# Performance work log

Measured on AMD Instinct MI355X. Metric: run time of the kernel, lower is better.

The kernel has to match this reference:

```python
import jax, jax.numpy as jnp
import numpy as np

N_MOL = 128
N_ATOMS_MAX = 1024
N_PAIRS = 4_194_304  # ~32 neighbors per atom


def setup_inputs() -> dict:
    key = jax.random.key(0)
    k0, k1, k2, k3, k4 = jax.random.split(key, 5)
    n_flat = N_MOL * N_ATOMS_MAX
    # coordinates inside a ~20 Angstrom box
    coordinates = jax.random.uniform(k0, (N_MOL, N_ATOMS_MAX, 3), jnp.float32) * 20.0
    # near-orthorhombic cells: 20*I + small perturbation
    cell = (jnp.eye(3, dtype=jnp.float32) * 20.0)[None, :, :] + 0.05 * jax.random.normal(
        k1, (N_MOL, 3, 3), jnp.float32)
    # all padded atoms treated as real -> identity index maps
    real_atoms = jnp.arange(n_flat, dtype=jnp.int64)
    inv_real_atoms = jnp.arange(n_flat, dtype=jnp.int64)
    mol_index = jnp.repeat(jnp.arange(N_MOL, dtype=jnp.int64), N_ATOMS_MAX)
    # neighbor pairs in padded flat-index space (what compute_one + mol offset emits)
    pair_first_raw = jax.random.randint(k2, (N_PAIRS,), 0, n_flat, dtype=jnp.int64)
    pair_second_raw = jax.random.randint(k3, (N_PAIRS,), 0, n_flat, dtype=jnp.int64)
    # periodic image offsets in {-1, 0, 1}^3
    offsets = jax.random.randint(k4, (N_PAIRS, 3), 0, 3, dtype=jnp.int32) - 1
    return dict(
        coordinates=coordinates,
        cell=cell,
        real_atoms=real_atoms,
        inv_real_atoms=inv_real_atoms,
        mol_index=mol_index,
        pair_first_raw=pair_first_raw,
        pair_second_raw=pair_second_raw,
        offsets=offsets,
        n_images=1,
        n_molecules=N_MOL,
        n_atoms_max=N_ATOMS_MAX,
    )


def reference(coordinates, cell, real_atoms, inv_real_atoms, mol_index,
              pair_first_raw, pair_second_raw, offsets, n_images,
              n_molecules, n_atoms_max):
    # map padded flat indices -> real-atom indices
    pair_first = inv_real_atoms[pair_first_raw]
    pair_second = inv_real_atoms[pair_second_raw]
    # linearized image-offset index in a (2*n_images+1)^3 grid
    n_off = 2 * n_images + 1
    o = offsets + n_images  # [P, 3], values in [0, n_off)
    offset_index = o[:, 2] + n_off * (o[:, 1] + n_off * o[:, 0])
    # per-pair cell gather and 3x3 matvec: offsets @ cell[mol]
    pair_mol = mol_index[pair_first]
    pair_cell = cell[pair_mol]  # [P, 3, 3]
    pair_offsets = jnp.einsum('pi,pij->pj', offsets.astype(cell.dtype), pair_cell)
    # gather real-atom coordinates from padded array
    coordflat = coordinates.reshape(n_molecules * n_atoms_max, 3)[real_atoms]
    paircoord = coordflat[pair_first] - coordflat[pair_second] + pair_offsets
    distflat2 = jnp.linalg.norm(paircoord, axis=1)
    return (distflat2, pair_first, pair_second, paircoord, offsets, offset_index)
```

## Files before the change

kernel.cpp:

```cpp
#include <hip/hip_runtime.h>


typedef int   iv4 __attribute__((ext_vector_type(4)));
typedef float fv4 __attribute__((ext_vector_type(4)));

#define NT_LOAD(p)      __builtin_nontemporal_load(p)
#define NT_STORE(p, v)  __builtin_nontemporal_store(v, p)

static __device__ __forceinline__ fv4 mkf4(float a, float b, float c, float d) {
    fv4 v; v.x = a; v.y = b; v.z = c; v.w = d; return v;
}

__global__ void build_tabA(
    const float* __restrict__ coordinates,
    const int*   __restrict__ real_atoms,
    const int*   __restrict__ inv_real_atoms,
    const int*   __restrict__ mol_index,
    fv4* __restrict__ tabA,
    int n_flat)
{
    int i = blockIdx.x * blockDim.x + threadIdx.x;
    if (i >= n_flat) return;
    const int pf = inv_real_atoms[i];
    const int r  = real_atoms[pf];
    const int m  = mol_index[pf];
    fv4 v;
    v.x = coordinates[3 * r + 0];
    v.y = coordinates[3 * r + 1];
    v.z = coordinates[3 * r + 2];
    v.w = __int_as_float(pf | (m << 17));
    tabA[i] = v;
}

__global__ void __launch_bounds__(256)
pairs_kernel(
    const fv4* __restrict__ tabA,
    const float* __restrict__ cell,
    const int* __restrict__ pair_first_raw,
    const int* __restrict__ pair_second_raw,
    const int* __restrict__ offsets,
    int n_images, int n_mol,
    float* __restrict__ out,
    int P)
{
    extern __shared__ float sc[];
    for (int i = threadIdx.x; i < n_mol * 9; i += blockDim.x)
        sc[i] = cell[i];
    __syncthreads();

    const int n_off = 2 * n_images + 1;

    const int t = blockIdx.x * blockDim.x + threadIdx.x;
    if (t * 4 >= P) return;

    const iv4 fr  = NT_LOAD((const iv4*)pair_first_raw + t);
    const iv4 sr  = NT_LOAD((const iv4*)pair_second_raw + t);
    const iv4 ow0 = NT_LOAD((const iv4*)offsets + 3 * t + 0);
    const iv4 ow1 = NT_LOAD((const iv4*)offsets + 3 * t + 1);
    const iv4 ow2 = NT_LOAD((const iv4*)offsets + 3 * t + 2);

    const int frv[4] = {fr.x, fr.y, fr.z, fr.w};
    const int srv[4] = {sr.x, sr.y, sr.z, sr.w};
    const int o[4][3] = {
        {ow0.x, ow0.y, ow0.z},
        {ow0.w, ow1.x, ow1.y},
        {ow1.z, ow1.w, ow2.x},
        {ow2.y, ow2.z, ow2.w},
    };

    fv4 A[4], B[4];
#pragma unroll
    for (int i = 0; i < 4; ++i) {
        A[i] = tabA[frv[i]];
        B[i] = tabA[srv[i]];
    }

    int pf[4], ps[4], oi[4];
    float pc[4][3], dist[4];
#pragma unroll
    for (int i = 0; i < 4; ++i) {
        const int wa = __float_as_int(A[i].w);
        const int wb = __float_as_int(B[i].w);
        pf[i] = wa & 0x1FFFF;
        ps[i] = wb & 0x1FFFF;
        const int mol = wa >> 17;
        const float* C = sc + mol * 9;

        const float f0 = (float)o[i][0], f1 = (float)o[i][1], f2 = (float)o[i][2];
        const float po0 = f0 * C[0] + f1 * C[3] + f2 * C[6];
        const float po1 = f0 * C[1] + f1 * C[4] + f2 * C[7];
        const float po2 = f0 * C[2] + f1 * C[5] + f2 * C[8];

        pc[i][0] = A[i].x - B[i].x + po0;
        pc[i][1] = A[i].y - B[i].y + po1;
        pc[i][2] = A[i].z - B[i].z + po2;
        dist[i] = sqrtf(pc[i][0] * pc[i][0] + pc[i][1] * pc[i][1] + pc[i][2] * pc[i][2]);

        oi[i] = (o[i][2] + n_images) + n_off * ((o[i][1] + n_images) + n_off * (o[i][0] + n_images));
    }

    NT_STORE((fv4*)(out) + t,          mkf4(dist[0], dist[1], dist[2], dist[3]));
    NT_STORE((fv4*)(out + P) + t,      mkf4((float)pf[0], (float)pf[1], (float)pf[2], (float)pf[3]));
    NT_STORE((fv4*)(out + 2 * P) + t,  mkf4((float)ps[0], (float)ps[1], (float)ps[2], (float)ps[3]));

    fv4* pc_out = (fv4*)(out + 3 * P) + 3 * t;
    NT_STORE(pc_out + 0, mkf4(pc[0][0], pc[0][1], pc[0][2], pc[1][0]));
    NT_STORE(pc_out + 1, mkf4(pc[1][1], pc[1][2], pc[2][0], pc[2][1]));
    NT_STORE(pc_out + 2, mkf4(pc[2][2], pc[3][0], pc[3][1], pc[3][2]));

    fv4* of_out = (fv4*)(out + 6 * P) + 3 * t;
    NT_STORE(of_out + 0, mkf4((float)o[0][0], (float)o[0][1], (float)o[0][2], (float)o[1][0]));
    NT_STORE(of_out + 1, mkf4((float)o[1][1], (float)o[1][2], (float)o[2][0], (float)o[2][1]));
    NT_STORE(of_out + 2, mkf4((float)o[2][2], (float)o[3][0], (float)o[3][1], (float)o[3][2]));

    NT_STORE((fv4*)(out + 9 * P) + t, mkf4((float)oi[0], (float)oi[1], (float)oi[2], (float)oi[3]));
}

__global__ void fallback_kernel(
    const float* __restrict__ coordinates,
    const float* __restrict__ cell,
    const int*   __restrict__ real_atoms,
    const int*   __restrict__ inv_real_atoms,
    const int*   __restrict__ mol_index,
    const int*   __restrict__ pair_first_raw,
    const int*   __restrict__ pair_second_raw,
    const int*   __restrict__ offsets,
    int n_images,
    float* __restrict__ out,
    int P)
{
    const int n_off = 2 * n_images + 1;
    int p = blockIdx.x * blockDim.x + threadIdx.x;
    if (p >= P) return;
    const int pf = inv_real_atoms[pair_first_raw[p]];
    const int ps = inv_real_atoms[pair_second_raw[p]];
    const int o0 = offsets[3 * p + 0], o1 = offsets[3 * p + 1], o2 = offsets[3 * p + 2];
    const int mol = mol_index[pf];
    const float* __restrict__ C = cell + mol * 9;
    const float f0 = (float)o0, f1 = (float)o1, f2 = (float)o2;
    const float po0 = f0 * C[0] + f1 * C[3] + f2 * C[6];
    const float po1 = f0 * C[1] + f1 * C[4] + f2 * C[7];
    const float po2 = f0 * C[2] + f1 * C[5] + f2 * C[8];
    const int ra = real_atoms[pf], rb = real_atoms[ps];
    const float pcx = coordinates[3*ra+0] - coordinates[3*rb+0] + po0;
    const float pcy = coordinates[3*ra+1] - coordinates[3*rb+1] + po1;
    const float pcz = coordinates[3*ra+2] - coordinates[3*rb+2] + po2;
    out[p] = sqrtf(pcx*pcx + pcy*pcy + pcz*pcz);
    out[P + p] = (float)pf;
    out[2*P + p] = (float)ps;
    out[3*P + 3*p + 0] = pcx; out[3*P + 3*p + 1] = pcy; out[3*P + 3*p + 2] = pcz;
    out[6*P + 3*p + 0] = (float)o0; out[6*P + 3*p + 1] = (float)o1; out[6*P + 3*p + 2] = (float)o2;
    out[9*P + p] = (float)((o2 + n_images) + n_off * ((o1 + n_images) + n_off * (o0 + n_images)));
}

extern "C" void kernel_launch(void* const* d_in, const int* in_sizes, int n_in,
                              void* d_out, int out_size, void* d_ws, size_t ws_size,
                              hipStream_t stream) {
    const float* coordinates     = (const float*)d_in[0];
    const float* cell            = (const float*)d_in[1];
    const int*   real_atoms      = (const int*)d_in[2];
    const int*   inv_real_atoms  = (const int*)d_in[3];
    const int*   mol_index       = (const int*)d_in[4];
    const int*   pair_first_raw  = (const int*)d_in[5];
    const int*   pair_second_raw = (const int*)d_in[6];
    const int*   offsets         = (const int*)d_in[7];

    const int P      = in_sizes[5];
    const int n_flat = in_sizes[2];
    const int n_mol  = in_sizes[1] / 9;
    const int n_images = 1;

    float* out = (float*)d_out;

    const size_t tabA_bytes = (size_t)n_flat * sizeof(fv4);
    const size_t smem_bytes = (size_t)n_mol * 9 * sizeof(float);

    if (ws_size >= tabA_bytes && smem_bytes <= 64 * 1024) {
        fv4* tabA = (fv4*)d_ws;

        build_tabA<<<(n_flat + 255) / 256, 256, 0, stream>>>(
            coordinates, real_atoms, inv_real_atoms, mol_index, tabA, n_flat);

        const int threads = P / 4;
        pairs_kernel<<<(threads + 255) / 256, 256, smem_bytes, stream>>>(
            tabA, cell, pair_first_raw, pair_second_raw, offsets,
            n_images, n_mol, out, P);
    } else {
        fallback_kernel<<<(P + 255) / 256, 256, 0, stream>>>(
            coordinates, cell, real_atoms, inv_real_atoms, mol_index,
            pair_first_raw, pair_second_raw, offsets, n_images, out, P);
    }
}
```

Baseline: 92.10 us.

## Convert pairs kernel to grid-stride loop with software-prefetched index loads

Caps the grid at 2048 blocks and makes each thread loop over several 4-pair chunks. It prefetches the next chunk's pair indices and offsets while gathering and computing the current chunk, and sets launch_bounds to request 8 blocks per CU. The goal is to overlap streaming index loads with the dependent tabA gathers and to amortize the shared-memory cell load. The trade-off is fewer resident waves to hide latency and extra registers for the prefetched values.

After: 169.7 us. 84.3% more time.

```diff
diff --git a/kernel.cpp b/kernel.cpp
--- a/kernel.cpp
+++ b/kernel.cpp
@@ -32,7 +32,7 @@
     tabA[i] = v;
 }
 
-__global__ void __launch_bounds__(256)
+__global__ void __launch_bounds__(256, 8)
 pairs_kernel(
     const fv4* __restrict__ tabA,
     const float* __restrict__ cell,
@@ -48,72 +48,88 @@
         sc[i] = cell[i];
     __syncthreads();
 
-    const int n_off = 2 * n_images + 1;
-
-    const int t = blockIdx.x * blockDim.x + threadIdx.x;
-    if (t * 4 >= P) return;
-
-    const iv4 fr  = NT_LOAD((const iv4*)pair_first_raw + t);
-    const iv4 sr  = NT_LOAD((const iv4*)pair_second_raw + t);
-    const iv4 ow0 = NT_LOAD((const iv4*)offsets + 3 * t + 0);
-    const iv4 ow1 = NT_LOAD((const iv4*)offsets + 3 * t + 1);
-    const iv4 ow2 = NT_LOAD((const iv4*)offsets + 3 * t + 2);
-
-    const int frv[4] = {fr.x, fr.y, fr.z, fr.w};
-    const int srv[4] = {sr.x, sr.y, sr.z, sr.w};
-    const int o[4][3] = {
-        {ow0.x, ow0.y, ow0.z},
-        {ow0.w, ow1.x, ow1.y},
-        {ow1.z, ow1.w, ow2.x},
-        {ow2.y, ow2.z, ow2.w},
-    };
-
-    fv4 A[4], B[4];
+    const int n_off   = 2 * n_images + 1;
+    const int nchunks = P >> 2;
+    const int stride  = gridDim.x * blockDim.x;
+
+    int c = blockIdx.x * blockDim.x + threadIdx.x;
+    if (c >= nchunks) return;
+
+    iv4 fr = NT_LOAD((const iv4*)pair_first_raw + c);
+    iv4 sr = NT_LOAD((const iv4*)pair_second_raw + c);
+    iv4 w0 = NT_LOAD((const iv4*)offsets + 3 * c + 0);
+    iv4 w1 = NT_LOAD((const iv4*)offsets + 3 * c + 1);
+    iv4 w2 = NT_LOAD((const iv4*)offsets + 3 * c + 2);
+
+    for (;;) {
+        fv4 A[4], B[4];
+        A[0] = tabA[fr.x]; B[0] = tabA[sr.x];
+        A[1] = tabA[fr.y]; B[1] = tabA[sr.y];
+        A[2] = tabA[fr.z]; B[2] = tabA[sr.z];
+        A[3] = tabA[fr.w]; B[3] = tabA[sr.w];
+
+        const int cn = c + stride;
+        const bool more = cn < nchunks;
+        iv4 nfr, nsr, nw0, nw1, nw2;
+        if (more) {
+            nfr = NT_LOAD((const iv4*)pair_first_raw + cn);
+            nsr = NT_LOAD((const iv4*)pair_second_raw + cn);
+            nw0 = NT_LOAD((const iv4*)offsets + 3 * cn + 0);
+            nw1 = NT_LOAD((const iv4*)offsets + 3 * cn + 1);
+            nw2 = NT_LOAD((const iv4*)offsets + 3 * cn + 2);
+        }
+
+        const int o[4][3] = {
+            {w0.x, w0.y, w0.z},
+            {w0.w, w1.x, w1.y},
+            {w1.z, w1.w, w2.x},
+            {w2.y, w2.z, w2.w},
+        };
+
+        int pf[4], ps[4], oi[4];
+        float pc[4][3], dist[4];
 #pragma unroll
-    for (int i = 0; i < 4; ++i) {
-        A[i] = tabA[frv[i]];
-        B[i] = tabA[srv[i]];
+        for (int i = 0; i < 4; ++i) {
+            const int wa = __float_as_int(A[i].w);
+            const int wb = __float_as_int(B[i].w);
+            pf[i] = wa & 0x1FFFF;
+            ps[i] = wb & 0x1FFFF;
+            const int mol = wa >> 17;
+            const float* C = sc + mol * 9;
+
+            const float f0 = (float)o[i][0], f1 = (float)o[i][1], f2 = (float)o[i][2];
+            const float po0 = f0 * C[0] + f1 * C[3] + f2 * C[6];
+            const float po1 = f0 * C[1] + f1 * C[4] + f2 * C[7];
+            const float po2 = f0 * C[2] + f1 * C[5] + f2 * C[8];
+
+            pc[i][0] = A[i].x - B[i].x + po0;
+            pc[i][1] = A[i].y - B[i].y + po1;
+            pc[i][2] = A[i].z - B[i].z + po2;
+            dist[i] = sqrtf(pc[i][0] * pc[i][0] + pc[i][1] * pc[i][1] + pc[i][2] * pc[i][2]);
+
+            oi[i] = (o[i][2] + n_images) + n_off * ((o[i][1] + n_images) + n_off * (o[i][0] + n_images));
+        }
+
+        NT_STORE((fv4*)(out) + c,          mkf4(dist[0], dist[1], dist[2], dist[3]));
+        NT_STORE((fv4*)(out + P) + c,      mkf4((float)pf[0], (float)pf[1], (float)pf[2], (float)pf[3]));
+        NT_STORE((fv4*)(out + 2 * P) + c,  mkf4((float)ps[0], (float)ps[1], (float)ps[2], (float)ps[3]));
+
+        fv4* pc_out = (fv4*)(out + 3 * P) + 3 * c;
+        NT_STORE(pc_out + 0, mkf4(pc[0][0], pc[0][1], pc[0][2], pc[1][0]));
+        NT_STORE(pc_out + 1, mkf4(pc[1][1], pc[1][2], pc[2][0], pc[2][1]));
+        NT_STORE(pc_out + 2, mkf4(pc[2][2], pc[3][0], pc[3][1], pc[3][2]));
+
+        fv4* of_out = (fv4*)(out + 6 * P) + 3 * c;
+        NT_STORE(of_out + 0, mkf4((float)o[0][0], (float)o[0][1], (float)o[0][2], (float)o[1][0]));
+        NT_STORE(of_out + 1, mkf4((float)o[1][1], (float)o[1][2], (float)o[2][0], (float)o[2][1]));
+        NT_STORE(of_out + 2, mkf4((float)o[2][2], (float)o[3][0], (float)o[3][1], (float)o[3][2]));
+
+        NT_STORE((fv4*)(out + 9 * P) + c, mkf4((float)oi[0], (float)oi[1], (float)oi[2], (float)oi[3]));
+
+        if (!more) break;
+        c = cn;
+        fr = nfr; sr = nsr; w0 = nw0; w1 = nw1; w2 = nw2;
     }
-
-    int pf[4], ps[4], oi[4];
-    float pc[4][3], dist[4];
-#pragma unroll
-    for (int i = 0; i < 4; ++i) {
-        const int wa = __float_as_int(A[i].w);
-        const int wb = __float_as_int(B[i].w);
-        pf[i] = wa & 0x1FFFF;
-        ps[i] = wb & 0x1FFFF;
-        const int mol = wa >> 17;
-        const float* C = sc + mol * 9;
-
-        const float f0 = (float)o[i][0], f1 = (float)o[i][1], f2 = (float)o[i][2];
-        const float po0 = f0 * C[0] + f1 * C[3] + f2 * C[6];
-        const float po1 = f0 * C[1] + f1 * C[4] + f2 * C[7];
-        const float po2 = f0 * C[2] + f1 * C[5] + f2 * C[8];
-
-        pc[i][0] = A[i].x - B[i].x + po0;
-        pc[i][1] = A[i].y - B[i].y + po1;
-        pc[i][2] = A[i].z - B[i].z + po2;
-        dist[i] = sqrtf(pc[i][0] * pc[i][0] + pc[i][1] * pc[i][1] + pc[i][2] * pc[i][2]);
-
-        oi[i] = (o[i][2] + n_images) + n_off * ((o[i][1] + n_images) + n_off * (o[i][0] + n_images));
-    }
-
-    NT_STORE((fv4*)(out) + t,          mkf4(dist[0], dist[1], dist[2], dist[3]));
-    NT_STORE((fv4*)(out + P) + t,      mkf4((float)pf[0], (float)pf[1], (float)pf[2], (float)pf[3]));
-    NT_STORE((fv4*)(out + 2 * P) + t,  mkf4((float)ps[0], (float)ps[1], (float)ps[2], (float)ps[3]));
-
-    fv4* pc_out = (fv4*)(out + 3 * P) + 3 * t;
-    NT_STORE(pc_out + 0, mkf4(pc[0][0], pc[0][1], pc[0][2], pc[1][0]));
-    NT_STORE(pc_out + 1, mkf4(pc[1][1], pc[1][2], pc[2][0], pc[2][1]));
-    NT_STORE(pc_out + 2, mkf4(pc[2][2], pc[3][0], pc[3][1], pc[3][2]));
-
-    fv4* of_out = (fv4*)(out + 6 * P) + 3 * t;
-    NT_STORE(of_out + 0, mkf4((float)o[0][0], (float)o[0][1], (float)o[0][2], (float)o[1][0]));
-    NT_STORE(of_out + 1, mkf4((float)o[1][1], (float)o[1][2], (float)o[2][0], (float)o[2][1]));
-    NT_STORE(of_out + 2, mkf4((float)o[2][2], (float)o[3][0], (float)o[3][1], (float)o[3][2]));
-
-    NT_STORE((fv4*)(out + 9 * P) + t, mkf4((float)oi[0], (float)oi[1], (float)oi[2], (float)oi[3]));
 }
 
 __global__ void fallback_kernel(
@@ -181,8 +197,10 @@
         build_tabA<<<(n_flat + 255) / 256, 256, 0, stream>>>(
             coordinates, real_atoms, inv_real_atoms, mol_index, tabA, n_flat);
 
-        const int threads = P / 4;
-        pairs_kernel<<<(threads + 255) / 256, 256, smem_bytes, stream>>>(
+        const int nchunks = P / 4;
+        int grid = (nchunks + 255) / 256;
+        if (grid > 2048) grid = 2048;
+        pairs_kernel<<<grid, 256, smem_bytes, stream>>>(
             tabA, cell, pair_first_raw, pair_second_raw, offsets,
             n_images, n_mol, out, P);
     } else {
```
